# Performance work log

Hardware: AMD Instinct MI355X
Metric: run time of the kernel (lower is better)

## Reference

```python
import jax, jax.numpy as jnp
import numpy as np

B, L, D, H = 4, 2048, 1024, 16
HD = D // H
EPS = 1e-5


def _layernorm(x, g, b):
    mu = jnp.mean(x, axis=-1, keepdims=True)
    var = jnp.mean(jnp.square(x - mu), axis=-1, keepdims=True)
    return (x - mu) * jax.lax.rsqrt(var + EPS) * g + b


def _rotate_half(x):
    x1, x2 = jnp.split(x, 2, axis=-1)
    return jnp.concatenate([-x2, x1], axis=-1)


def setup_inputs() -> dict:
    key = jax.random.key(0)
    ks = jax.random.split(key, 12)
    s = 0.02
    return {
        "x": jax.random.normal(ks[0], (B, L, D), jnp.float32),
        "pos_cos": jax.random.uniform(ks[1], (B, L, D), jnp.float32),
        "pos_sin": jax.random.uniform(ks[2], (B, L, D), jnp.float32),
        "attn_mask": jnp.zeros((B, L), jnp.float32),
        "Wq": jax.random.normal(ks[3], (D, D), jnp.float32) * s,
        "Wk": jax.random.normal(ks[4], (D, D), jnp.float32) * s,
        "Wv": jax.random.normal(ks[5], (D, D), jnp.float32) * s,
        "Wo": jax.random.normal(ks[6], (D, D), jnp.float32) * s,
        "W1": jax.random.normal(ks[7], (D, 2 * D), jnp.float32) * s,
        "W2": jax.random.normal(ks[8], (D, D), jnp.float32) * s,
        "g1": jnp.ones((D,), jnp.float32),
        "b1": jnp.zeros((D,), jnp.float32),
        "g2": jnp.ones((D,), jnp.float32),
        "b2": jnp.zeros((D,), jnp.float32),
    }


def reference(x, pos_cos, pos_sin, attn_mask, Wq, Wk, Wv, Wo, W1, W2, g1, b1, g2, b2):
    # --- attention sublayer (pre-LN) ---
    residual = x
    xn = _layernorm(x, g1, b1)
    split_heads = lambda t: t.reshape(B, L, H, HD).transpose(0, 2, 1, 3)  # [B,H,L,hd]
    q = split_heads(xn @ Wq)
    k = split_heads(xn @ Wk)
    v = split_heads(xn @ Wv)
    cos = split_heads(pos_cos)
    sin = split_heads(pos_sin)
    q = q * cos + _rotate_half(q) * sin
    k = k * cos + _rotate_half(k) * sin
    scores = jnp.einsum('bhqd,bhkd->bhqk', q, k) / np.float32(np.sqrt(HD))
    scores = scores + attn_mask[:, None, None, :]  # additive mask over keys
    probs = jax.nn.softmax(scores, axis=-1)
    ctx = jnp.einsum('bhqk,bhkd->bhqd', probs, v)
    ctx = ctx.transpose(0, 2, 1, 3).reshape(B, L, D)
    x = residual + ctx @ Wo
    # --- SwiGLU FFN sublayer (pre-LN) ---
    residual = x
    xn = _layernorm(x, g2, b2)
    h = xn @ W1
    x1, x2 = h[..., :D], h[..., D:]
    ffn = (jax.nn.silu(x1) * x2) @ W2
    return residual + ffn
```

## Files before the change

kernel.cpp:

```cpp
#include <hip/hip_runtime.h>
#include <hip/hip_bf16.h>

typedef unsigned short ushort_t;
typedef short short8 __attribute__((ext_vector_type(8)));
typedef unsigned short u16x4 __attribute__((ext_vector_type(4)));
typedef float f32x4 __attribute__((ext_vector_type(4)));
typedef int int2v __attribute__((ext_vector_type(2)));
typedef int int4v __attribute__((ext_vector_type(4)));

#define MFMA_BF16 __builtin_amdgcn_mfma_f32_16x16x32_bf16

#define GLDS16(g, l) __builtin_amdgcn_global_load_lds( \
    (__attribute__((address_space(1))) void*)(g), \
    (__attribute__((address_space(3))) void*)(l), 16, 0, 0)

__device__ __forceinline__ unsigned short f2bf(float f) {
  union { float f; unsigned u; } v; v.f = f;
  unsigned r = v.u + 0x7FFFu + ((v.u >> 16) & 1u);
  return (unsigned short)(r >> 16);
}
__device__ __forceinline__ float bf2f(unsigned short h) {
  union { unsigned u; float f; } v; v.u = ((unsigned)h) << 16;
  return v.f;
}
__device__ __forceinline__ unsigned pack_bf2(float a, float b) {
  __hip_bfloat162 t = __float22bfloat162_rn(float2{a, b});
  union { __hip_bfloat162 h; unsigned u; } v; v.h = t;
  return v.u;
}
__device__ __forceinline__ float exp2_raw(float x) {
  float r;
  asm volatile("v_exp_f32 %0, %1" : "=v"(r) : "v"(x));
  return r;
}

#define BB 4
#define LL 2048
#define DD 1024
#define HH 16
#define HD 64
#define NROW (BB * LL)
#define LOG2E 1.4426950408889634f

template <int PERM>
__global__ __launch_bounds__(256) void wconv(const float* __restrict__ W,
                                             ushort_t* __restrict__ WT,
                                             int R, int C) {
  __shared__ float tile[32][33];
  const int ct = blockIdx.x * 32, rt = blockIdx.y * 32;
  const int tx = threadIdx.x & 31, ty = threadIdx.x >> 5;
#pragma unroll
  for (int j = 0; j < 4; ++j)
    tile[ty + j * 8][tx] = W[(size_t)(rt + ty + j * 8) * C + ct + tx];
  __syncthreads();
  int orow0 = ct;
  if (PERM)
    orow0 = (ct < 1024) ? ((ct >> 5) * 64) : ((((ct - 1024) >> 5) * 64) + 32);
#pragma unroll
  for (int j = 0; j < 4; ++j)
    WT[(size_t)(orow0 + ty + j * 8) * R + rt + tx] = f2bf(tile[tx][ty + j * 8]);
}

__global__ void mask_scale(const float* __restrict__ mask,
                           float* __restrict__ maskl) {
  const int i = blockIdx.x * 256 + threadIdx.x;
  maskl[i] = mask[i] * LOG2E;
}

template <int BIN>
__global__ __launch_bounds__(256) void ln_kernel(const void* __restrict__ xin,
                                                 const float* __restrict__ g,
                                                 const float* __restrict__ bt,
                                                 ushort_t* __restrict__ out) {
  const int row = blockIdx.x, t = threadIdx.x;
  f32x4 v;
  if (BIN) {
    const u16x4 hv =
        *(const u16x4*)((const ushort_t*)xin + (size_t)row * DD + t * 4);
    v[0] = bf2f(hv[0]); v[1] = bf2f(hv[1]);
    v[2] = bf2f(hv[2]); v[3] = bf2f(hv[3]);
  } else {
    v = *(const f32x4*)((const float*)xin + (size_t)row * DD + t * 4);
  }
  float s = v[0] + v[1] + v[2] + v[3];
  float sq = v[0] * v[0] + v[1] * v[1] + v[2] * v[2] + v[3] * v[3];
#pragma unroll
  for (int off = 1; off < 64; off <<= 1) {
    s += __shfl_xor(s, off);
    sq += __shfl_xor(sq, off);
  }
  __shared__ float aw[4], aq[4];
  if ((t & 63) == 0) { aw[t >> 6] = s; aq[t >> 6] = sq; }
  __syncthreads();
  s = aw[0] + aw[1] + aw[2] + aw[3];
  sq = aq[0] + aq[1] + aq[2] + aq[3];
  const float mu = s * (1.f / DD);
  const float var = sq * (1.f / DD) - mu * mu;
  const float rs = rsqrtf(var + 1e-5f);
  u16x4 o;
#pragma unroll
  for (int j = 0; j < 4; ++j) {
    const int c = t * 4 + j;
    o[j] = f2bf((v[j] - mu) * rs * g[c] + bt[c]);
  }
  *(u16x4*)(out + (size_t)row * DD + t * 4) = o;
}

template <int EPI>
__global__ __launch_bounds__(256) void gemm64(
    const ushort_t* __restrict__ A, const ushort_t* __restrict__ BT,
    const float* __restrict__ pcos, const float* __restrict__ psin,
    ushort_t* __restrict__ qh, ushort_t* __restrict__ kh,
    ushort_t* __restrict__ vt, ushort_t* __restrict__ gact,
    ushort_t* __restrict__ Cb, float* __restrict__ Cf,
    const float* __restrict__ residf, const ushort_t* __restrict__ residb,
    int M, int N, int K) {
  __shared__ ushort_t As[128 * 64];
  __shared__ ushort_t Bs[128 * 64];
  const int tid = threadIdx.x;
  const int lane = tid & 63;
  const int w = tid >> 6;
  const int wr = w >> 1, wc = w & 1;
  const int orig = blockIdx.y * gridDim.x + blockIdx.x;
  const int xcd = orig & 7;
  const int lid = orig >> 3;
  const int bm = (xcd * 8 + (lid & 7)) * 128;
  const int bn = (lid >> 3) * 128;
  const int fr = lane & 15;
  const int hi = lane >> 4;
  const int srow8 = lane >> 3;
  const int schunk = (lane & 7) ^ srow8;
  f32x4 acc[4][4];
#pragma unroll
  for (int m = 0; m < 4; ++m)
#pragma unroll
    for (int n = 0; n < 4; ++n) acc[m][n] = (f32x4){0.f, 0.f, 0.f, 0.f};

  const int nk = K >> 6;
  for (int kt = 0; kt < nk; ++kt) {
    __syncthreads();
#pragma unroll
    for (int c = 0; c < 4; ++c) {
      const int rbase = w * 32 + c * 8;
      const int grow = rbase + srow8;
      GLDS16(A + (size_t)(bm + grow) * K + kt * 64 + schunk * 8,
             &As[rbase * 64]);
      GLDS16(BT + (size_t)(bn + grow) * K + kt * 64 + schunk * 8,
             &Bs[rbase * 64]);
    }
    asm volatile("s_waitcnt vmcnt(0)" ::: "memory");
    __syncthreads();
#pragma unroll
    for (int khf = 0; khf < 2; ++khf) {
      short8 af[4], bf_[4];
#pragma unroll
      for (int m = 0; m < 4; ++m) {
        const int r = wr * 64 + m * 16 + fr;
        af[m] = *(const short8*)&As[r * 64 + (((khf << 2) + hi) ^ (fr & 7)) * 8];
      }
#pragma unroll
      for (int n = 0; n < 4; ++n) {
        const int r = wc * 64 + n * 16 + fr;
        bf_[n] = *(const short8*)&Bs[r * 64 + (((khf << 2) + hi) ^ (fr & 7)) * 8];
      }
#pragma unroll
      for (int m = 0; m < 4; ++m)
#pragma unroll
        for (int n = 0; n < 4; ++n)
          acc[m][n] = MFMA_BF16(af[m], bf_[n], acc[m][n], 0, 0, 0);
    }
  }

  if (EPI == 1) {
    const int gcol = bn + wc * 64;
    const int region = gcol >> 10;
    const int h = (gcol & 1023) >> 6;
    const int b = bm >> 11;
    if (region < 2) {
      const float qs = (region == 0) ? (0.125f * LOG2E) : 1.0f;
      ushort_t* dstbuf = (region == 0) ? qh : kh;
      const int dbase = h * 64;
#pragma unroll
      for (int m = 0; m < 4; ++m) {
        const int gr0 = bm + wr * 64 + m * 16 + hi * 4;
#pragma unroll
        for (int r = 0; r < 4; ++r) {
          const int gr = gr0 + r;
          const int l = gr & 2047;
          const float* pcr = pcos + (size_t)gr * DD + dbase;
          const float* psr = psin + (size_t)gr * DD + dbase;
          ushort_t* dst = dstbuf + ((size_t)(b * HH + h) * LL + l) * HD;
#pragma unroll
          for (int n = 0; n < 2; ++n) {
            const int dlo = n * 16 + fr;
            const float xlo = acc[m][n][r], xhi = acc[m][n + 2][r];
            dst[dlo] = f2bf((xlo * pcr[dlo] - xhi * psr[dlo]) * qs);
            dst[dlo + 32] = f2bf((xhi * pcr[dlo + 32] + xlo * psr[dlo + 32]) * qs);
          }
        }
      }
    } else {
      const size_t bhv = (size_t)(b * HH + h);
      const int l0 = (bm & 2047) + wr * 64;
      const int lt = l0 >> 6;
#pragma unroll
      for (int m = 0; m < 4; ++m) {
        const int slotb = 32 * (m >> 1) + 8 * hi + 4 * (m & 1);
#pragma unroll
        for (int n = 0; n < 4; ++n) {
          const int hd = n * 16 + fr;
          u16x4 wv;
          wv[0] = f2bf(acc[m][n][0]);
          wv[1] = f2bf(acc[m][n][1]);
          wv[2] = f2bf(acc[m][n][2]);
          wv[3] = f2bf(acc[m][n][3]);
          *(u16x4*)(vt + (bhv * HD + hd) * LL + lt * 64 + slotb) = wv;
        }
      }
    }
  } else if (EPI == 2) {
    const int jbase = ((bn + wc * 64) >> 6) * 32;
#pragma unroll
    for (int m = 0; m < 4; ++m) {
      const int gr0 = bm + wr * 64 + m * 16 + hi * 4;
#pragma unroll
      for (int r = 0; r < 4; ++r) {
        ushort_t* dst = gact + (size_t)(gr0 + r) * DD + jbase;
#pragma unroll
        for (int n = 0; n < 2; ++n) {
          const float x1 = acc[m][n][r];
          const float x2 = acc[m][n + 2][r];
          dst[n * 16 + fr] = f2bf(x1 / (1.f + __expf(-x1)) * x2);
        }
      }
    }
  } else {
#pragma unroll
    for (int m = 0; m < 4; ++m)
#pragma unroll
      for (int n = 0; n < 4; ++n)
#pragma unroll
        for (int r = 0; r < 4; ++r) {
          const int gr = bm + wr * 64 + m * 16 + hi * 4 + r;
          const int gc = bn + wc * 64 + n * 16 + fr;
          const size_t o = (size_t)gr * N + gc;
          if (EPI == 3) Cb[o] = f2bf(residf[o] + acc[m][n][r]);
          else          Cf[o] = bf2f(residb[o]) + acc[m][n][r];
        }
  }
}

__global__ __launch_bounds__(512) void attn_kernel(
    const ushort_t* __restrict__ qh, const ushort_t* __restrict__ kh,
    const ushort_t* __restrict__ vt, const float* __restrict__ maskl,
    ushort_t* __restrict__ ctx) {
  const int tid = threadIdx.x, lane = tid & 63, w = tid >> 6;
  const int bh = blockIdx.y, b = bh >> 4, h = bh & 15;
  const int q0 = blockIdx.x * 128;
  __shared__ ushort_t Ks[2][64 * 64];
  __shared__ ushort_t Vs[2][64 * 64];
  const int fr = lane & 15;
  const int hi = lane >> 4;
  const int fo = hi * 8;
  const int qrow = q0 + w * 16 + fr;
  const size_t qoff = ((size_t)bh * LL + qrow) * HD + fo;
  const short8 qf0 = *(const short8*)(qh + qoff);
  const short8 qf1 = *(const short8*)(qh + qoff + 32);
  short8 ones;
#pragma unroll
  for (int i = 0; i < 8; ++i) ones[i] = (short)0x3F80;

  f32x4 oacc[4];
  f32x4 lacc = (f32x4){0.f, 0.f, 0.f, 0.f};
#pragma unroll
  for (int m = 0; m < 4; ++m) oacc[m] = (f32x4){0.f, 0.f, 0.f, 0.f};

  const int lrow = lane >> 3;
  const int lcs = ((lane & 7) ^ lrow) * 8;
  const int rr = w * 8 + lrow;

  const float* mrow = maskl + (size_t)b * LL;

  const int NT = LL / 128;
  for (int kt = 0; kt < NT; ++kt) {
    __syncthreads();
    GLDS16(kh + ((size_t)bh * LL + kt * 128 + rr) * HD + lcs, &Ks[0][w * 512]);
    GLDS16(kh + ((size_t)bh * LL + kt * 128 + 64 + rr) * HD + lcs,
           &Ks[1][w * 512]);
    GLDS16(vt + ((size_t)bh * HD + rr) * LL + kt * 128 + lcs, &Vs[0][w * 512]);
    GLDS16(vt + ((size_t)bh * HD + rr) * LL + kt * 128 + 64 + lcs,
           &Vs[1][w * 512]);
    f32x4 mk[8];
#pragma unroll
    for (int n = 0; n < 8; ++n)
      mk[n] = *(const f32x4*)(mrow + kt * 128 + n * 16 + hi * 4);
    asm volatile("s_waitcnt vmcnt(0)" ::: "memory");
    __syncthreads();

#pragma unroll
    for (int sub = 0; sub < 2; ++sub) {
      f32x4 s[4];
#pragma unroll
      for (int n = 0; n < 4; ++n) s[n] = mk[sub * 4 + n];
      __builtin_amdgcn_s_setprio(1);
#pragma unroll
      for (int n = 0; n < 4; ++n) {
        const int krow = n * 16 + fr;
#pragma unroll
        for (int c = 0; c < 2; ++c) {
          const int col = (c * 32 + fo) ^ ((fr & 7) * 8);
          const short8 kf = *(const short8*)&Ks[sub][krow * 64 + col];
          s[n] = MFMA_BF16(kf, c ? qf1 : qf0, s[n], 0, 0, 0);
        }
      }
      __builtin_amdgcn_s_setprio(0);
      unsigned pk[4][2];
#pragma unroll
      for (int n = 0; n < 4; ++n) {
        const float p0 = exp2_raw(s[n][0]);
        const float p1 = exp2_raw(s[n][1]);
        const float p2 = exp2_raw(s[n][2]);
        const float p3 = exp2_raw(s[n][3]);
        pk[n][0] = pack_bf2(p0, p1);
        pk[n][1] = pack_bf2(p2, p3);
      }
      __builtin_amdgcn_s_setprio(1);
#pragma unroll
      for (int c = 0; c < 2; ++c) {
        int4v pw = {(int)pk[2 * c][0], (int)pk[2 * c][1],
                    (int)pk[2 * c + 1][0], (int)pk[2 * c + 1][1]};
        union { int4v i; short8 s; } pf; pf.i = pw;
#pragma unroll
        for (int m = 0; m < 4; ++m) {
          const int row = m * 16 + fr;
          const int col = (c * 32 + fo) ^ ((fr & 7) * 8);
          const short8 vf = *(const short8*)&Vs[sub][row * 64 + col];
          oacc[m] = MFMA_BF16(vf, pf.s, oacc[m], 0, 0, 0);
        }
        lacc = MFMA_BF16(ones, pf.s, lacc, 0, 0, 0);
      }
      __builtin_amdgcn_s_setprio(0);
    }
  }
  const float inv = 1.f / lacc[0];
  const int q = q0 + w * 16 + fr;
  ushort_t* dst = ctx + ((size_t)b * LL + q) * DD + h * 64 + hi * 4;
#pragma unroll
  for (int m = 0; m < 4; ++m) {
    int2v val;
    val[0] = (int)pack_bf2(oacc[m][0] * inv, oacc[m][1] * inv);
    val[1] = (int)pack_bf2(oacc[m][2] * inv, oacc[m][3] * inv);
    *(int2v*)(dst + m * 16) = val;
  }
}

extern "C" void kernel_launch(void* const* d_in, const int* in_sizes, int n_in,
                              void* d_out, int out_size, void* d_ws,
                              size_t ws_size, hipStream_t stream) {
  const float* x = (const float*)d_in[0];
  const float* pcos = (const float*)d_in[1];
  const float* psin = (const float*)d_in[2];
  const float* mask = (const float*)d_in[3];
  const float* Wq = (const float*)d_in[4];
  const float* Wk = (const float*)d_in[5];
  const float* Wv = (const float*)d_in[6];
  const float* Wo = (const float*)d_in[7];
  const float* W1 = (const float*)d_in[8];
  const float* W2 = (const float*)d_in[9];
  const float* g1 = (const float*)d_in[10];
  const float* b1 = (const float*)d_in[11];
  const float* g2 = (const float*)d_in[12];
  const float* b2 = (const float*)d_in[13];
  float* out = (float*)d_out;
  char* ws = (char*)d_ws;

  ushort_t* WQKVT = (ushort_t*)(ws);
  ushort_t* WOT = (ushort_t*)(ws + 6291456);
  ushort_t* W1T = (ushort_t*)(ws + 8388608);
  ushort_t* W2T = (ushort_t*)(ws + 12582912);
  ushort_t* XN = (ushort_t*)(ws + 14680064);
  float* MASKL = (float*)(ws + 31457280);
  ushort_t* GACT = (ushort_t*)(ws + 31457280 + 33554432);
  ushort_t* QH = (ushort_t*)(ws + 81788928);
  ushort_t* KH = (ushort_t*)(ws + 98566144);
  ushort_t* VT = (ushort_t*)(ws + 115343360);
  ushort_t* CTX = (ushort_t*)(ws + 132120576);
  ushort_t* XMIDB = (ushort_t*)(ws + 148897792);

  wconv<0><<<dim3(32, 32), 256, 0, stream>>>(Wq, WQKVT, 1024, 1024);
  wconv<0><<<dim3(32, 32), 256, 0, stream>>>(Wk, WQKVT + 1024 * 1024, 1024, 1024);
  wconv<0><<<dim3(32, 32), 256, 0, stream>>>(Wv, WQKVT + 2 * 1024 * 1024, 1024, 1024);
  wconv<0><<<dim3(32, 32), 256, 0, stream>>>(Wo, WOT, 1024, 1024);
  wconv<1><<<dim3(64, 32), 256, 0, stream>>>(W1, W1T, 1024, 2048);
  wconv<0><<<dim3(32, 32), 256, 0, stream>>>(W2, W2T, 1024, 1024);
  mask_scale<<<(BB * LL) / 256, 256, 0, stream>>>(mask, MASKL);

  ln_kernel<0><<<NROW, 256, 0, stream>>>(x, g1, b1, XN);
  gemm64<1><<<dim3(24, 64), 256, 0, stream>>>(
      XN, WQKVT, pcos, psin, QH, KH, VT, nullptr, nullptr, nullptr, nullptr,
      nullptr, NROW, 3072, 1024);
  attn_kernel<<<dim3(16, 64), 512, 0, stream>>>(QH, KH, VT, MASKL, CTX);
  gemm64<3><<<dim3(8, 64), 256, 0, stream>>>(
      CTX, WOT, nullptr, nullptr, nullptr, nullptr, nullptr, nullptr, XMIDB,
      nullptr, x, nullptr, NROW, 1024, 1024);
  ln_kernel<1><<<NROW, 256, 0, stream>>>(XMIDB, g2, b2, XN);
  gemm64<2><<<dim3(16, 64), 256, 0, stream>>>(
      XN, W1T, nullptr, nullptr, nullptr, nullptr, nullptr, GACT, nullptr,
      nullptr, nullptr, nullptr, NROW, 2048, 1024);
  gemm64<4><<<dim3(8, 64), 256, 0, stream>>>(
      GACT, W2T, nullptr, nullptr, nullptr, nullptr, nullptr, nullptr, nullptr,
      out, nullptr, XMIDB, NROW, 1024, 1024);
}
```

Before: 331.2 us.

## Stage QK RoPE epilogue through LDS for vectorized stores; remap attention blocks per XCD

The Q/K projection epilogue now writes accumulators as bf16 into a padded LDS tile per wave. Each lane then owns one row and applies RoPE with vectorized float4 cos/sin loads and 16-byte bf16 stores, replacing scattered 2-byte stores and strided scalar loads. The attention kernel's block index is also remapped so all query tiles of one (batch, head) land on the same XCD, improving L2 reuse of K/V. The change adds a barrier, an LDS round trip and a bf16 rounding of the pre-RoPE values, which slightly changes numerics.

```diff
diff --git a/kernel.cpp b/kernel.cpp
--- a/kernel.cpp
+++ b/kernel.cpp
@@ -41,6 +41,7 @@
 #define HD 64
 #define NROW (BB * LL)
 #define LOG2E 1.4426950408889634f
+#define EPAD 68
 
 template <int PERM>
 __global__ __launch_bounds__(256) void wconv(const float* __restrict__ W,
@@ -115,8 +116,9 @@
     ushort_t* __restrict__ Cb, float* __restrict__ Cf,
     const float* __restrict__ residf, const ushort_t* __restrict__ residb,
     int M, int N, int K) {
-  __shared__ ushort_t As[128 * 64];
-  __shared__ ushort_t Bs[128 * 64];
+  __shared__ ushort_t smem[4 * 64 * EPAD];
+  ushort_t* As = smem;
+  ushort_t* Bs = smem + 128 * 64;
   const int tid = threadIdx.x;
   const int lane = tid & 63;
   const int w = tid >> 6;
@@ -176,28 +178,53 @@
     const int region = gcol >> 10;
     const int h = (gcol & 1023) >> 6;
     const int b = bm >> 11;
+    __syncthreads();
     if (region < 2) {
+      ushort_t* Es = smem + w * 64 * EPAD;
+#pragma unroll
+      for (int m = 0; m < 4; ++m)
+#pragma unroll
+        for (int n = 0; n < 4; ++n)
+#pragma unroll
+          for (int r = 0; r < 4; ++r)
+            Es[(m * 16 + hi * 4 + r) * EPAD + n * 16 + fr] =
+                f2bf(acc[m][n][r]);
+      asm volatile("s_waitcnt lgkmcnt(0)" ::: "memory");
+      __builtin_amdgcn_sched_barrier(0);
+      const int rl = lane;
       const float qs = (region == 0) ? (0.125f * LOG2E) : 1.0f;
-      ushort_t* dstbuf = (region == 0) ? qh : kh;
-      const int dbase = h * 64;
-#pragma unroll
-      for (int m = 0; m < 4; ++m) {
-        const int gr0 = bm + wr * 64 + m * 16 + hi * 4;
-#pragma unroll
-        for (int r = 0; r < 4; ++r) {
-          const int gr = gr0 + r;
-          const int l = gr & 2047;
-          const float* pcr = pcos + (size_t)gr * DD + dbase;
-          const float* psr = psin + (size_t)gr * DD + dbase;
-          ushort_t* dst = dstbuf + ((size_t)(b * HH + h) * LL + l) * HD;
-#pragma unroll
-          for (int n = 0; n < 2; ++n) {
-            const int dlo = n * 16 + fr;
-            const float xlo = acc[m][n][r], xhi = acc[m][n + 2][r];
-            dst[dlo] = f2bf((xlo * pcr[dlo] - xhi * psr[dlo]) * qs);
-            dst[dlo + 32] = f2bf((xhi * pcr[dlo + 32] + xlo * psr[dlo + 32]) * qs);
-          }
-        }
+      const int gr = bm + wr * 64 + rl;
+      const int l = gr & 2047;
+      const float* pc = pcos + (size_t)gr * DD + h * 64;
+      const float* ps = psin + (size_t)gr * DD + h * 64;
+      ushort_t* dst = ((region == 0) ? qh : kh) +
+                      ((size_t)(b * HH + h) * LL + l) * HD;
+#pragma unroll
+      for (int d0 = 0; d0 < 32; d0 += 8) {
+        const u16x4 a0 = *(const u16x4*)&Es[rl * EPAD + d0];
+        const u16x4 a1 = *(const u16x4*)&Es[rl * EPAD + d0 + 4];
+        const u16x4 b0 = *(const u16x4*)&Es[rl * EPAD + d0 + 32];
+        const u16x4 b1 = *(const u16x4*)&Es[rl * EPAD + d0 + 36];
+        const f32x4 cl0 = *(const f32x4*)(pc + d0);
+        const f32x4 cl1 = *(const f32x4*)(pc + d0 + 4);
+        const f32x4 ch0 = *(const f32x4*)(pc + d0 + 32);
+        const f32x4 ch1 = *(const f32x4*)(pc + d0 + 36);
+        const f32x4 sl0 = *(const f32x4*)(ps + d0);
+        const f32x4 sl1 = *(const f32x4*)(ps + d0 + 4);
+        const f32x4 sh0 = *(const f32x4*)(ps + d0 + 32);
+        const f32x4 sh1 = *(const f32x4*)(ps + d0 + 36);
+        short8 olo, ohi;
+#pragma unroll
+        for (int j = 0; j < 4; ++j) {
+          const float xl0 = bf2f(a0[j]), xh0 = bf2f(b0[j]);
+          const float xl1 = bf2f(a1[j]), xh1 = bf2f(b1[j]);
+          olo[j] = (short)f2bf((xl0 * cl0[j] - xh0 * sl0[j]) * qs);
+          olo[j + 4] = (short)f2bf((xl1 * cl1[j] - xh1 * sl1[j]) * qs);
+          ohi[j] = (short)f2bf((xh0 * ch0[j] + xl0 * sh0[j]) * qs);
+          ohi[j + 4] = (short)f2bf((xh1 * ch1[j] + xl1 * sh1[j]) * qs);
+        }
+        *(short8*)(dst + d0) = olo;
+        *(short8*)(dst + d0 + 32) = ohi;
       }
     } else {
       const size_t bhv = (size_t)(b * HH + h);
@@ -255,8 +282,12 @@
     const ushort_t* __restrict__ vt, const float* __restrict__ maskl,
     ushort_t* __restrict__ ctx) {
   const int tid = threadIdx.x, lane = tid & 63, w = tid >> 6;
-  const int bh = blockIdx.y, b = bh >> 4, h = bh & 15;
-  const int q0 = blockIdx.x * 128;
+  const int flat = blockIdx.y * gridDim.x + blockIdx.x;
+  const int xcd = flat & 7;
+  const int slot = flat >> 3;
+  const int bh = xcd * 8 + (slot >> 4);
+  const int q0 = (slot & 15) * 128;
+  const int b = bh >> 4, h = bh & 15;
   __shared__ ushort_t Ks[2][64 * 64];
   __shared__ ushort_t Vs[2][64 * 64];
   const int fr = lane & 15;
```

New measurement: 357.1 us. 7.8% more time.
